# Optimization experiments

Measured on AMD Instinct MI355X. Metric: run time of the kernel, lower is better.

## Reference

```python
import jax, jax.numpy as jnp
import numpy as np

N, C_IN, H, W = 256, 256, 28, 28
D = 64        # prototype channel dim (prototype_shape[1])
P = 200       # num prototypes
NCLS = 10


def setup_inputs() -> dict:
    key = jax.random.key(0)
    ks = jax.random.split(key, 6)
    x = jax.random.normal(ks[0], (N, C_IN, H, W), dtype=jnp.float32)
    W1 = jax.random.normal(ks[1], (D, C_IN), dtype=jnp.float32) * 0.05
    b1 = jnp.zeros((D,), dtype=jnp.float32)
    W2 = jax.random.normal(ks[2], (D, D), dtype=jnp.float32) * 0.05
    b2 = jnp.zeros((D,), dtype=jnp.float32)
    prototypes = jax.random.uniform(ks[3], (P, D), dtype=jnp.float32)
    last_W = jax.random.normal(ks[4], (NCLS, P), dtype=jnp.float32) * 0.05
    last_b = jnp.zeros((NCLS,), dtype=jnp.float32)
    return {"x": x, "W1": W1, "b1": b1, "W2": W2, "b2": b2,
            "prototypes": prototypes, "last_W": last_W, "last_b": last_b}


def reference(x, W1, b1, W2, b2, prototypes, last_W, last_b):
    # add_on_layers: 1x1 conv -> relu -> 1x1 conv -> sigmoid (pointwise GEMMs)
    h = jax.nn.relu(jnp.einsum('nchw,oc->nohw', x, W1) + b1[None, :, None, None])
    f = jax.nn.sigmoid(jnp.einsum('nchw,oc->nohw', h, W2) + b2[None, :, None, None])
    # L2 convolution with 1x1 prototypes:
    # conv(x^2, ones) == channel sum of f^2, broadcast over P prototypes
    x2_patch_sum = jnp.sum(f * f, axis=1, keepdims=True)          # (N,1,H,W)
    xp = jnp.einsum('nchw,pc->nphw', f, prototypes)               # (N,P,H,W)
    p2 = jnp.sum(prototypes * prototypes, axis=1)[None, :, None, None]  # (1,P,1,1)
    distances = jax.nn.relu(x2_patch_sum - 2.0 * xp + p2)         # (N,P,H,W)
    # global min-pool over spatial dims (== -maxpool(-d) with full kernel)
    min_distances = jnp.min(distances, axis=(2, 3))               # (N,P)
    # paf == 'linear': similarity = -distance
    prototype_activations = -min_distances
    logits = prototype_activations @ last_W.T + last_b            # (N,NCLS)
    return (logits, min_distances)
```

## Files before the change

kernel.cpp:

```cpp
#include <hip/hip_runtime.h>
#include <hip/hip_bf16.h>

#define NIMG 256
#define CIN  256
#define PIX  784
#define DD   64
#define NP   200
#define NPP  208
#define NCLS 10

#define XS 264
#define HS 72

typedef __attribute__((ext_vector_type(8))) short bf16x8;
typedef __attribute__((ext_vector_type(4))) float f32x4;
typedef __attribute__((ext_vector_type(4))) unsigned int u32x4;
typedef __attribute__((ext_vector_type(2))) unsigned int u32x2;

__device__ __forceinline__ unsigned short f2bf(float f) {
    union { float f; unsigned int u; } v; v.f = f;
    unsigned int r = v.u + 0x7fffu + ((v.u >> 16) & 1u);
    return (unsigned short)(r >> 16);
}
__device__ __forceinline__ unsigned int pk2(float a, float b) {
    __hip_bfloat162 p = __float22bfloat162_rn(make_float2(a, b));
    return *(unsigned int*)&p;
}

#define MFMA(a, b, c) __builtin_amdgcn_mfma_f32_16x16x32_bf16((a), (b), (c), 0, 0, 0)

#define BARL() asm volatile("s_waitcnt lgkmcnt(0)\n\ts_barrier" ::: "memory")

__global__ __launch_bounds__(1024, 4)
void proto_fused_kernel(const float* __restrict__ x,
                        const float* __restrict__ W1, const float* __restrict__ b1,
                        const float* __restrict__ W2, const float* __restrict__ b2,
                        const float* __restrict__ proto,
                        const float* __restrict__ lastW, const float* __restrict__ lastb,
                        float* __restrict__ out)
{
    __shared__ __align__(16) unsigned short xlds[64 * XS];
    __shared__ __align__(16) unsigned short w1lds[64 * XS];
    __shared__ __align__(16) unsigned short htile[64 * HS];
    __shared__ __align__(16) unsigned short ftile[64 * HS];
    __shared__ float p2lds[NPP];
    __shared__ float s2lds[4][64];
    __shared__ float b1lds[DD], b2lds[DD];
    __shared__ unsigned int bmin[NPP];

    const int n    = blockIdx.x;
    const int t    = threadIdx.x;
    const int lane = t & 63;
    const int q    = lane >> 4;
    const int l15  = lane & 15;
    const int wave = t >> 6;
    const int s    = wave & 3;
    const int dt   = wave >> 2;

    const int p4  = ((t >> 2) & 15) * 4;
    const int c4i = (t & 3) | ((t >> 6) << 2);
    const int c4  = c4i * 4;
    const float* xn = x + (size_t)n * CIN * PIX;

    auto load_st = [&](float4 (&pf)[4], int st) {
        const int base = st * 64 + p4;
        #pragma unroll
        for (int j = 0; j < 4; ++j) {
            const float* src = xn + (size_t)(c4 + j) * PIX + base;
            float4 v;
            if (base + 3 < PIX) {
                v = *(const float4*)src;
            } else {
                v.x = (base + 0 < PIX) ? src[0] : 0.f;
                v.y = (base + 1 < PIX) ? src[1] : 0.f;
                v.z = (base + 2 < PIX) ? src[2] : 0.f;
                v.w = (base + 3 < PIX) ? src[3] : 0.f;
            }
            pf[j] = v;
        }
    };
    auto store_st = [&](float4 (&pf)[4]) {
        #pragma unroll
        for (int r = 0; r < 4; ++r) {
            u32x2 w;
            w.x = pk2(((const float*)&pf[0])[r], ((const float*)&pf[1])[r]);
            w.y = pk2(((const float*)&pf[2])[r], ((const float*)&pf[3])[r]);
            *(u32x2*)&xlds[(p4 + r) * XS + c4] = w;
        }
    };

    float4 pfA[4], pfB[4], pfC[4];
    load_st(pfA, 0);
    load_st(pfB, 1);
    load_st(pfC, 2);

    {
        const float4* W1v = (const float4*)W1;
        #pragma unroll
        for (int i = 0; i < 4; ++i) {
            int j = t + i * 1024;
            float4 v = W1v[j];
            u32x2 w;
            w.x = pk2(v.x, v.y); w.y = pk2(v.z, v.w);
            *(u32x2*)&w1lds[(j >> 6) * XS + (j & 63) * 4] = w;
        }
    }
    if (t < DD) { b1lds[t] = b1[t]; b2lds[t] = b2[t]; }
    if (t < NPP) {
        float acc = 0.f;
        if (t < NP) {
            const float4* pp = (const float4*)(proto + t * DD);
            #pragma unroll
            for (int i = 0; i < 16; ++i) {
                float4 v = pp[i];
                acc += v.x * v.x + v.y * v.y + v.z * v.z + v.w * v.w;
            }
        }
        p2lds[t] = acc;
        bmin[t] = 0x7f800000u;
    }

    bf16x8 w2f[2];
    #pragma unroll
    for (int kk = 0; kk < 2; ++kk) {
        const float4* src = (const float4*)(W2 + (size_t)(dt * 16 + l15) * DD + kk * 32 + q * 8);
        float4 a = src[0], b = src[1];
        union { u32x4 u; bf16x8 h; } cv;
        cv.u.x = pk2(a.x, a.y); cv.u.y = pk2(a.z, a.w);
        cv.u.z = pk2(b.x, b.y); cv.u.w = pk2(b.z, b.w);
        w2f[kk] = cv.h;
    }

    bf16x8 pb0[4], pb1[4];
    #pragma unroll
    for (int it = 0; it < 4; ++it) {
        int pt = dt + 4 * it;
        int p  = pt * 16 + l15;
        int pr = (p < NP) ? p : (NP - 1);
        const float4* src = (const float4*)(proto + (size_t)pr * DD + q * 8);
        float4 a = src[0], b = src[1];
        float4 c = src[8], d = src[9];
        union { u32x4 u; bf16x8 h; } cv0, cv1;
        cv0.u.x = pk2(a.x, a.y); cv0.u.y = pk2(a.z, a.w);
        cv0.u.z = pk2(b.x, b.y); cv0.u.w = pk2(b.z, b.w);
        cv1.u.x = pk2(c.x, c.y); cv1.u.y = pk2(c.z, c.w);
        cv1.u.z = pk2(d.x, d.y); cv1.u.w = pk2(d.z, d.w);
        pb0[it] = cv0.h; pb1[it] = cv1.h;
    }

    store_st(pfA);
    load_st(pfA, 3);
    BARL();

    float p2r[4];
    #pragma unroll
    for (int it = 0; it < 4; ++it) {
        int pidx = (dt + 4 * it) * 16 + l15;
        p2r[it] = p2lds[pidx < NPP ? pidx : (NPP - 1)];
    }

    float rmin[4];
    #pragma unroll
    for (int it = 0; it < 4; ++it) rmin[it] = 1e30f;

    const int arow  = (s * 16 + l15) * XS + q * 8;
    const int wrow  = (dt * 16 + l15) * XS + q * 8;
    const int arowH = (s * 16 + l15) * HS + q * 8;
    const int bidx  = dt * 16 + l15;

    auto ITER = [&](int st, float4 (&pf)[4]) {
        {
            f32x4 acc = {0.f, 0.f, 0.f, 0.f};
            #pragma unroll
            for (int kk = 0; kk < 8; ++kk) {
                bf16x8 a = *(const bf16x8*)&xlds[arow + kk * 32];
                bf16x8 w = *(const bf16x8*)&w1lds[wrow + kk * 32];
                acc = MFMA(a, w, acc);
            }
            #pragma unroll
            for (int r = 0; r < 4; ++r) {
                int prow = s * 16 + q * 4 + r;
                float h = fmaxf(acc[r] + b1lds[bidx], 0.f);
                htile[prow * HS + bidx] = f2bf(h);
            }
        }
        BARL();

        if (st < 12) {
            store_st(pf);
            if (st <= 8) load_st(pf, st + 4);
        }
        {
            f32x4 acc = {0.f, 0.f, 0.f, 0.f};
            bf16x8 a0 = *(const bf16x8*)&htile[arowH];
            bf16x8 a1 = *(const bf16x8*)&htile[arowH + 32];
            acc = MFMA(a0, w2f[0], acc);
            acc = MFMA(a1, w2f[1], acc);
            #pragma unroll
            for (int r = 0; r < 4; ++r) {
                int prow = s * 16 + q * 4 + r;
                float z = acc[r] + b2lds[bidx];
                float f = __builtin_amdgcn_rcpf(1.0f + __builtin_amdgcn_exp2f(z * -1.44269504f));
                ftile[prow * HS + bidx] = f2bf(f);
                float v = f * f;
                v += __shfl_xor(v, 1, 64);
                v += __shfl_xor(v, 2, 64);
                v += __shfl_xor(v, 4, 64);
                v += __shfl_xor(v, 8, 64);
                if (l15 == 0)
                    s2lds[dt][prow] = (st * 64 + prow < PIX) ? v : 1e30f;
            }
        }
        BARL();

        {
            bf16x8 a0 = *(const bf16x8*)&ftile[arowH];
            bf16x8 a1 = *(const bf16x8*)&ftile[arowH + 32];
            float s2v[4];
            #pragma unroll
            for (int r = 0; r < 4; ++r) {
                int pl = s * 16 + q * 4 + r;
                s2v[r] = (s2lds[0][pl] + s2lds[1][pl]) + (s2lds[2][pl] + s2lds[3][pl]);
            }
            #pragma unroll
            for (int it = 0; it < 4; ++it) {
                int pt = dt + 4 * it;
                if (pt < 13) {
                    f32x4 acc = {0.f, 0.f, 0.f, 0.f};
                    acc = MFMA(a0, pb0[it], acc);
                    acc = MFMA(a1, pb1[it], acc);
                    float m = 1e30f;
                    #pragma unroll
                    for (int r = 0; r < 4; ++r) {
                        float dist = fmaxf(s2v[r] - 2.f * acc[r] + p2r[it], 0.f);
                        m = fminf(m, dist);
                    }
                    rmin[it] = fminf(rmin[it], m);
                }
            }
        }
    };

    for (int base = 0; base < 15; base += 3) {
        if (base + 0 < 13) ITER(base + 0, pfB);
        if (base + 1 < 13) ITER(base + 1, pfC);
        if (base + 2 < 13) ITER(base + 2, pfA);
    }

    #pragma unroll
    for (int it = 0; it < 4; ++it) {
        int pt = dt + 4 * it;
        if (pt < 13) {
            float m = rmin[it];
            m = fminf(m, __shfl_xor(m, 16, 64));
            m = fminf(m, __shfl_xor(m, 32, 64));
            if (lane < 16) atomicMin(&bmin[pt * 16 + l15], __float_as_uint(m));
        }
    }
    BARL();

    if (t < NP) {
        out[NIMG * NCLS + (size_t)n * NP + t] = __uint_as_float(bmin[t]);
    }
    if (t < 320) {
        int c = t >> 5, j = t & 31;
        float acc = 0.f;
        for (int p = j; p < NP; p += 32)
            acc += __uint_as_float(bmin[p]) * lastW[c * NP + p];
        acc += __shfl_xor(acc, 1, 32);
        acc += __shfl_xor(acc, 2, 32);
        acc += __shfl_xor(acc, 4, 32);
        acc += __shfl_xor(acc, 8, 32);
        acc += __shfl_xor(acc, 16, 32);
        if (j == 0) out[(size_t)n * NCLS + c] = -acc + lastb[c];
    }
}

extern "C" void kernel_launch(void* const* d_in, const int* in_sizes, int n_in,
                              void* d_out, int out_size, void* d_ws, size_t ws_size,
                              hipStream_t stream) {
    const float* x     = (const float*)d_in[0];
    const float* W1    = (const float*)d_in[1];
    const float* b1    = (const float*)d_in[2];
    const float* W2    = (const float*)d_in[3];
    const float* b2    = (const float*)d_in[4];
    const float* proto = (const float*)d_in[5];
    const float* lastW = (const float*)d_in[6];
    const float* lastb = (const float*)d_in[7];
    float* out = (float*)d_out;

    proto_fused_kernel<<<dim3(NIMG), dim3(1024), 0, stream>>>(
        x, W1, b1, W2, b2, proto, lastW, lastb, out);
}
```

Baseline: 352.2 us.

## Move prototype fragments to LDS and shorten prefetch ring to cut registers

```diff
diff --git a/kernel.cpp b/kernel.cpp
--- a/kernel.cpp
+++ b/kernel.cpp
@@ -7,6 +7,7 @@
 #define DD   64
 #define NP   200
 #define NPP  208
+#define NPT  13
 #define NCLS 10
 
 #define XS 264
@@ -31,7 +32,7 @@
 
 #define BARL() asm volatile("s_waitcnt lgkmcnt(0)\n\ts_barrier" ::: "memory")
 
-__global__ __launch_bounds__(1024, 4)
+__global__ __launch_bounds__(1024, 1)
 void proto_fused_kernel(const float* __restrict__ x,
                         const float* __restrict__ W1, const float* __restrict__ b1,
                         const float* __restrict__ W2, const float* __restrict__ b2,
@@ -43,6 +44,7 @@
     __shared__ __align__(16) unsigned short w1lds[64 * XS];
     __shared__ __align__(16) unsigned short htile[64 * HS];
     __shared__ __align__(16) unsigned short ftile[64 * HS];
+    __shared__ __align__(16) unsigned short pblds[NPT * 2 * 64 * 8];
     __shared__ float p2lds[NPP];
     __shared__ float s2lds[4][64];
     __shared__ float b1lds[DD], b2lds[DD];
@@ -89,10 +91,9 @@
         }
     };
 
-    float4 pfA[4], pfB[4], pfC[4];
+    float4 pfA[4], pfB[4];
     load_st(pfA, 0);
     load_st(pfB, 1);
-    load_st(pfC, 2);
 
     {
         const float4* W1v = (const float4*)W1;
@@ -103,6 +104,17 @@
             u32x2 w;
             w.x = pk2(v.x, v.y); w.y = pk2(v.z, v.w);
             *(u32x2*)&w1lds[(j >> 6) * XS + (j & 63) * 4] = w;
+        }
+    }
+    {
+        #pragma unroll
+        for (int i = 0; i < 13; ++i) {
+            int idx = t + i * 1024;
+            int p = idx >> 6, k = idx & 63;
+            float v = (p < NP) ? proto[p * DD + k] : 0.f;
+            int pt = p >> 4, l = p & 15, half = k >> 5, qq = (k & 31) >> 3, k7 = k & 7;
+            if (pt < NPT)
+                pblds[(((pt * 2 + half) * 4 + qq) * 16 + l) * 8 + k7] = f2bf(v);
         }
     }
     if (t < DD) { b1lds[t] = b1[t]; b2lds[t] = b2[t]; }
@@ -131,25 +143,8 @@
         w2f[kk] = cv.h;
     }
 
-    bf16x8 pb0[4], pb1[4];
-    #pragma unroll
-    for (int it = 0; it < 4; ++it) {
-        int pt = dt + 4 * it;
-        int p  = pt * 16 + l15;
-        int pr = (p < NP) ? p : (NP - 1);
-        const float4* src = (const float4*)(proto + (size_t)pr * DD + q * 8);
-        float4 a = src[0], b = src[1];
-        float4 c = src[8], d = src[9];
-        union { u32x4 u; bf16x8 h; } cv0, cv1;
-        cv0.u.x = pk2(a.x, a.y); cv0.u.y = pk2(a.z, a.w);
-        cv0.u.z = pk2(b.x, b.y); cv0.u.w = pk2(b.z, b.w);
-        cv1.u.x = pk2(c.x, c.y); cv1.u.y = pk2(c.z, c.w);
-        cv1.u.z = pk2(d.x, d.y); cv1.u.w = pk2(d.z, d.w);
-        pb0[it] = cv0.h; pb1[it] = cv1.h;
-    }
-
     store_st(pfA);
-    load_st(pfA, 3);
+    load_st(pfA, 2);
     BARL();
 
     float p2r[4];
@@ -167,6 +162,7 @@
     const int wrow  = (dt * 16 + l15) * XS + q * 8;
     const int arowH = (s * 16 + l15) * HS + q * 8;
     const int bidx  = dt * 16 + l15;
+    const int pboff = (q * 16 + l15) * 8;
 
     auto ITER = [&](int st, float4 (&pf)[4]) {
         {
@@ -188,7 +184,7 @@
 
         if (st < 12) {
             store_st(pf);
-            if (st <= 8) load_st(pf, st + 4);
+            if (st <= 9) load_st(pf, st + 3);
         }
         {
             f32x4 acc = {0.f, 0.f, 0.f, 0.f};
@@ -225,10 +221,12 @@
             #pragma unroll
             for (int it = 0; it < 4; ++it) {
                 int pt = dt + 4 * it;
-                if (pt < 13) {
+                if (pt < NPT) {
+                    bf16x8 b0 = *(const bf16x8*)&pblds[(pt * 2 + 0) * 512 + pboff];
+                    bf16x8 b1v = *(const bf16x8*)&pblds[(pt * 2 + 1) * 512 + pboff];
                     f32x4 acc = {0.f, 0.f, 0.f, 0.f};
-                    acc = MFMA(a0, pb0[it], acc);
-                    acc = MFMA(a1, pb1[it], acc);
+                    acc = MFMA(a0, b0, acc);
+                    acc = MFMA(a1, b1v, acc);
                     float m = 1e30f;
                     #pragma unroll
                     for (int r = 0; r < 4; ++r) {
@@ -241,16 +239,15 @@
         }
     };
 
-    for (int base = 0; base < 15; base += 3) {
-        if (base + 0 < 13) ITER(base + 0, pfB);
-        if (base + 1 < 13) ITER(base + 1, pfC);
-        if (base + 2 < 13) ITER(base + 2, pfA);
+    for (int stp = 0; stp < 13; stp += 2) {
+        ITER(stp, pfB);
+        if (stp + 1 < 13) ITER(stp + 1, pfA);
     }
 
     #pragma unroll
     for (int it = 0; it < 4; ++it) {
         int pt = dt + 4 * it;
-        if (pt < 13) {
+        if (pt < NPT) {
             float m = rmin[it];
             m = fminf(m, __shfl_xor(m, 16, 64));
             m = fminf(m, __shfl_xor(m, 32, 64));
```

Measured after the change: 308.3 us. 12.5% less time.
